# Optimization experiments

Hardware: AMD Instinct MI355X
Metric: run time of the kernel (lower is better)

## Reference

```python
import jax, jax.numpy as jnp
import numpy as np
from jax import lax

NUM_CHANNELS = 3
NUM_HEADS = 8
PATCH = 16  # projection_dim = 3 * 16 * 16 = 768
EPS = 1e-5


def setup_inputs() -> dict:
    key = jax.random.key(0)
    ks = jax.random.split(key, 16)
    B, N, D, Hdim = 4, 1024, 768, 3072
    H = NUM_HEADS

    def init(k, shape, fan_in):
        bound = 1.0 / np.sqrt(fan_in)
        return jax.random.uniform(k, shape, jnp.float32, -bound, bound)

    return {
        "x": jax.random.normal(ks[0], (B, N, D), jnp.float32),
        # 3x3 conv QKV projections over per-patch [3,16,16] images (no bias, qkv_bias=False)
        "qconv_w": init(ks[1], (NUM_CHANNELS, NUM_CHANNELS, 3, 3), NUM_CHANNELS * 9),
        "kconv_w": init(ks[2], (NUM_CHANNELS, NUM_CHANNELS, 3, 3), NUM_CHANNELS * 9),
        "vconv_w": init(ks[3], (NUM_CHANNELS, NUM_CHANNELS, 3, 3), NUM_CHANNELS * 9),
        # 1x1 conv mixing heads of the attention map + BatchNorm2d(heads)
        "reatten_w": init(ks[4], (H, H), H),
        "reatten_b": init(ks[5], (H,), H),
        "bn_g": jnp.ones((H,), jnp.float32),
        "bn_b": jnp.zeros((H,), jnp.float32),
        # output projection (Linear dim->dim)
        "proj_w": init(ks[6], (D, D), D),
        "proj_b": init(ks[7], (D,), D),
        # LayerNorm over (num_patches, projection_dim) jointly
        "ln_g": jnp.ones((N, D), jnp.float32),
        "ln_b": jnp.zeros((N, D), jnp.float32),
        # FeedForward
        "ff_w1": init(ks[8], (Hdim, D), D),
        "ff_b1": init(ks[9], (Hdim,), D),
        "ff_w2": init(ks[10], (D, Hdim), Hdim),
        "ff_b2": init(ks[11], (D,), Hdim),
    }


def _conv3x3(x, w):
    # x: [BN, C, p, p], w: [C, C, 3, 3], stride 1, SAME padding
    return lax.conv_general_dilated(x, w, (1, 1), "SAME",
                                    dimension_numbers=("NCHW", "OIHW", "NCHW"))


def _layernorm_2d(x, g, b):
    # LayerNorm over last two axes (N, D) jointly, biased variance, eps=1e-5
    mu = jnp.mean(x, axis=(-2, -1), keepdims=True)
    var = jnp.mean(jnp.square(x - mu), axis=(-2, -1), keepdims=True)
    return (x - mu) * lax.rsqrt(var + EPS) * g + b


def _encoder_fwd(x, qconv_w, kconv_w, vconv_w, reatten_w, reatten_b,
                 bn_g, bn_b, proj_w, proj_b, ln_g, ln_b,
                 ff_w1, ff_b1, ff_w2, ff_b2):
    B, N, D = x.shape
    H = NUM_HEADS
    hd = D // H
    scale = hd ** -0.5

    # --- ReAttention ---
    xi = x.reshape(B * N, NUM_CHANNELS, PATCH, PATCH)

    def qkv(w):
        y = _conv3x3(xi, w).reshape(B, N, H, hd)
        return y.transpose(0, 2, 1, 3)  # [B, H, N, hd]

    q, k, v = qkv(qconv_w), qkv(kconv_w), qkv(vconv_w)

    attn = jax.nn.softmax(jnp.einsum("bhnd,bhmd->bhnm", q, k) * scale, axis=-1)

    # learned cross-head 1x1 conv + BatchNorm2d (training-mode batch stats)
    attn = jnp.einsum("gh,bhnm->bgnm", reatten_w, attn) + reatten_b[None, :, None, None]
    mu = jnp.mean(attn, axis=(0, 2, 3), keepdims=True)
    var = jnp.mean(jnp.square(attn - mu), axis=(0, 2, 3), keepdims=True)
    attn = (attn - mu) * lax.rsqrt(var + EPS)
    attn = attn * bn_g[None, :, None, None] + bn_b[None, :, None, None]

    out = jnp.einsum("bhnm,bhmd->bhnd", attn, v)
    out = out.transpose(0, 2, 1, 3).reshape(B, N, D)
    out = out @ proj_w.T + proj_b

    # --- residual + LN ---
    x1 = _layernorm_2d(x + out, ln_g, ln_b)

    # --- FeedForward (exact GELU) + residual + LN ---
    h = jax.nn.gelu(x1 @ ff_w1.T + ff_b1, approximate=False)
    ff = h @ ff_w2.T + ff_b2
    return _layernorm_2d(x1 + ff, ln_g, ln_b)


def reference(x, qconv_w, kconv_w, vconv_w, reatten_w, reatten_b,
              bn_g, bn_b, proj_w, proj_b, ln_g, ln_b,
              ff_w1, ff_b1, ff_w2, ff_b2):
    return _encoder_fwd(x, qconv_w, kconv_w, vconv_w, reatten_w, reatten_b,
                        bn_g, bn_b, proj_w, proj_b, ln_g, ln_b,
                        ff_w1, ff_b1, ff_w2, ff_b2)
```

## Files before the change

kernel.cpp:

```cpp
#include <hip/hip_runtime.h>
#include <math.h>


typedef unsigned short u16;
typedef unsigned int u32;
typedef __bf16 bf16x8 __attribute__((ext_vector_type(8)));
typedef float f32x4 __attribute__((ext_vector_type(4)));

#define EPSV 1e-5f
#define SL2E 0.14724444620253177f
#define EXPC -11.541560327111707f

__device__ __forceinline__ u16 f2bf(float f) {
  union { float f; u32 u; } v; v.f = f;
  u32 u = v.u + 0x7fffu + ((v.u >> 16) & 1u);
  return (u16)(u >> 16);
}
__device__ __forceinline__ float bf2f(u16 h) {
  union { u32 u; float f; } v; v.u = ((u32)h) << 16; return v.f;
}
__device__ __forceinline__ f32x4 mfma16(bf16x8 a, bf16x8 b, f32x4 c) {
  return __builtin_amdgcn_mfma_f32_16x16x32_bf16(a, b, c, 0, 0, 0);
}
__device__ __forceinline__ void gload16(const void* gp, void* lp) {
  __builtin_amdgcn_global_load_lds(
      (const __attribute__((address_space(1))) u32*)gp,
      (__attribute__((address_space(3))) u32*)lp, 16, 0, 0);
}

struct KS { int off[3]; int hl[3]; };
__device__ __forceinline__ KS ks_init(int t) {
  KS ks;
  int lane = t & 63;
  int lh = lane >> 4, l15 = lane & 15;
  #pragma unroll
  for (int j = 0; j < 3; ++j) {
    int G = j * 512 + t;
    int hl = (G >= 768) ? 1 : 0;
    int C = (G - hl * 768) >> 6;
    int chunk = C / 6, r = C - 6 * chunk;
    int kk = r >> 1, c1 = r & 1;
    int m = chunk * 32 + ((l15 >> 2) << 3) + (c1 << 2) + (l15 & 3);
    ks.off[j] = m * 96 + kk * 32 + lh * 8;
    ks.hl[j] = hl;
  }
  return ks;
}
__device__ __forceinline__ void ks_stage(const u16* __restrict__ khi,
    const u16* __restrict__ klo, size_t rowel, const KS& ks, u16* Kb, int t) {
  int w = t >> 6;
  #pragma unroll
  for (int j = 0; j < 3; ++j) {
    const u16* src = (ks.hl[j] ? klo : khi) + rowel + ks.off[j];
    gload16(src, Kb + (size_t)(j * 512 + w * 64) * 8);
  }
}

__device__ __forceinline__ void qload(const u16* __restrict__ qhi,
    const u16* __restrict__ qlo, size_t qoff, bf16x8* qh, bf16x8* ql) {
  #pragma unroll
  for (int kk = 0; kk < 3; ++kk) {
    qh[kk] = *(const bf16x8*)(qhi + qoff + kk * 32);
    ql[kk] = *(const bf16x8*)(qlo + qoff + kk * 32);
  }
}

__device__ __forceinline__ void score18(const u16* Kb, int mh, int lane,
    const bf16x8* qh, const bf16x8* ql, f32x4& C0, f32x4& C1) {
  C0 = (f32x4){0.f, 0.f, 0.f, 0.f};
  C1 = (f32x4){0.f, 0.f, 0.f, 0.f};
  #pragma unroll
  for (int kk = 0; kk < 3; ++kk) {
    const u16* base = Kb + (mh * 6 + kk * 2) * 512 + lane * 8;
    bf16x8 kh0 = *(const bf16x8*)(base);
    bf16x8 kh1 = *(const bf16x8*)(base + 512);
    bf16x8 kl0 = *(const bf16x8*)(base + 6144);
    bf16x8 kl1 = *(const bf16x8*)(base + 6656);
    C0 = mfma16(kh0, qh[kk], C0);
    C0 = mfma16(kl0, qh[kk], C0);
    C0 = mfma16(kh0, ql[kk], C0);
    C1 = mfma16(kh1, qh[kk], C1);
    C1 = mfma16(kl1, qh[kk], C1);
    C1 = mfma16(kh1, ql[kk], C1);
  }
}

__global__ __launch_bounds__(256) void k_f2b(const float* __restrict__ s,
                                             u16* __restrict__ d, int n) {
  int i = blockIdx.x * 256 + threadIdx.x;
  int stride = gridDim.x * 256;
  for (; i < n; i += stride) d[i] = f2bf(s[i]);
}

__global__ __launch_bounds__(256) void k_conv(const float* __restrict__ x,
    const float* __restrict__ wq, const float* __restrict__ wk, const float* __restrict__ wv,
    u16* __restrict__ qhi, u16* __restrict__ qlo,
    u16* __restrict__ khi, u16* __restrict__ klo,
    float* __restrict__ vb)
{
  __shared__ float patch[768], swq[81], swk[81], swv[81];
  int bid = blockIdx.x;
  int b = bid >> 10, n = bid & 1023;
  int t = threadIdx.x;
  const float* xr = x + (size_t)bid * 768;
  patch[t] = xr[t]; patch[t + 256] = xr[t + 256]; patch[t + 512] = xr[t + 512];
  if (t < 81) { swq[t] = wq[t]; swk[t] = wk[t]; swv[t] = wv[t]; }
  __syncthreads();
  #pragma unroll
  for (int r = 0; r < 3; ++r) {
    int f = t + 256 * r;
    int o = f >> 8, rem = f & 255, pp = rem >> 4, qq = rem & 15;
    float aq = 0.f, ak = 0.f, av = 0.f;
    #pragma unroll
    for (int i = 0; i < 3; ++i)
      #pragma unroll
      for (int dp = 0; dp < 3; ++dp) {
        int ip = pp + dp - 1;
        if (ip < 0 || ip > 15) continue;
        #pragma unroll
        for (int dq = 0; dq < 3; ++dq) {
          int iq = qq + dq - 1;
          if (iq < 0 || iq > 15) continue;
          float pv = patch[i * 256 + ip * 16 + iq];
          int wi = ((o * 3 + i) * 3 + dp) * 3 + dq;
          aq += swq[wi] * pv; ak += swk[wi] * pv; av += swv[wi] * pv;
        }
      }
    int h = f / 96, d = f - h * 96;
    size_t oi = ((size_t)(b * 8 + h) * 1024 + n) * 96 + d;
    float aqs = aq * SL2E;
    u16 qh_ = f2bf(aqs); qhi[oi] = qh_; qlo[oi] = f2bf(aqs - bf2f(qh_));
    u16 kh_ = f2bf(ak);  khi[oi] = kh_; klo[oi] = f2bf(ak - bf2f(kh_));
    vb[oi] = av;
  }
}

__global__ __launch_bounds__(256) void k_vtr(const float* __restrict__ vb,
                                             u16* __restrict__ vtr)
{
  __shared__ u16 lds[12288];
  int bid = blockIdx.x;
  int bh = bid >> 3, n0 = (bid & 7) * 128;
  int t = threadIdx.x;
  int n = t >> 1, dh = (t & 1) * 48;
  const float* src = vb + ((size_t)bh * 1024 + n0 + n) * 96 + dh;
  #pragma unroll
  for (int j4 = 0; j4 < 12; ++j4) {
    float4 v = *(const float4*)(src + j4 * 4);
    int d = dh + j4 * 4;
    lds[(d + 0) * 128 + n] = f2bf(v.x);
    lds[(d + 1) * 128 + n] = f2bf(v.y);
    lds[(d + 2) * 128 + n] = f2bf(v.z);
    lds[(d + 3) * 128 + n] = f2bf(v.w);
  }
  __syncthreads();
  #pragma unroll
  for (int j = 0; j < 48; ++j) {
    int flat = t + 256 * j;
    int d = flat >> 7, n2 = flat & 127;
    vtr[((size_t)bh * 96 + d) * 1024 + n0 + n2] = lds[flat];
  }
}

__global__ __launch_bounds__(512, 2) void k_score(
    const u16* __restrict__ qhi, const u16* __restrict__ qlo,
    const u16* __restrict__ khi, const u16* __restrict__ klo,
    float* __restrict__ zp, u16* __restrict__ pt)
{
  __shared__ u16 Kst[2][12288];
  int p = blockIdx.x;
  int s = p >> 3;
  int c = (p & 7) * 4 + (s >> 4);
  int ng = s & 15;
  int b = c >> 3, mg = c & 7;
  int t = threadIdx.x, lane = t & 63, w = t >> 6;
  int l15 = lane & 15, lhi = lane >> 4;
  int nsub = w >> 1, mh = w & 1;
  int n0 = ng * 64 + nsub * 16;
  int nt = ng * 4 + nsub;
  int m0base = mg * 128;
  KS ks = ks_init(t);
  bf16x8 qh[3], ql[3], qh2[3], ql2[3];
  size_t bh0 = (size_t)(b * 8) * 1024;
  ks_stage(khi, klo, (bh0 + m0base) * 96, ks, Kst[0], t);
  qload(qhi, qlo, (bh0 + n0 + l15) * 96 + lhi * 8, qh, ql);
  __syncthreads();
  #pragma unroll 1
  for (int h = 0; h < 8; ++h) {
    float z = 0.f;
    #pragma unroll
    for (int mt = 0; mt < 2; ++mt) {
      int u = h * 2 + mt;
      if (u < 15) {
        int un = u + 1, hn = un >> 1, mtn = un & 1;
        size_t bhn = (size_t)(b * 8 + hn) * 1024;
        ks_stage(khi, klo, (bhn + m0base + mtn * 64) * 96, ks, Kst[(u + 1) & 1], t);
        if (mtn == 0)
          qload(qhi, qlo, (bhn + n0 + l15) * 96 + lhi * 8, qh2, ql2);
      }
      f32x4 C0, C1;
      score18(Kst[u & 1], mh, lane, qh, ql, C0, C1);
      union { u16 us[8]; uint4 q4; } pk;
      #pragma unroll
      for (int r = 0; r < 4; ++r) {
        float e0 = exp2f(C0[r] + EXPC);
        float e1 = exp2f(C1[r] + EXPC);
        z += e0 + e1;
        pk.us[r]     = f2bf(e0);
        pk.us[4 + r] = f2bf(e1);
      }
      int mc = mg * 4 + mt * 2 + mh;
      *(uint4*)&pt[((((size_t)(b * 8 + h) * 32 + mc) * 64 + nt) * 64 + lane) * 8] = pk.q4;
      if (u < 15 && mt == 1) {
        #pragma unroll
        for (int kk = 0; kk < 3; ++kk) { qh[kk] = qh2[kk]; ql[kk] = ql2[kk]; }
      }
      __syncthreads();
    }
    z += __shfl_xor(z, 16);
    z += __shfl_xor(z, 32);
    if (lane < 16)
      zp[((size_t)((b * 8 + h) * 16 + mg * 2 + mh)) * 1024 + n0 + lane] = z;
  }
}

__global__ __launch_bounds__(256) void k_zmerge(const float* __restrict__ zp,
                                                float* __restrict__ invZ)
{
  int idx = blockIdx.x * 256 + threadIdx.x;
  int bh = idx >> 10, n = idx & 1023;
  float z = 0.f;
  #pragma unroll
  for (int s = 0; s < 16; ++s) z += zp[((size_t)(bh * 16 + s)) * 1024 + n];
  invZ[idx] = 1.f / z;
}

__global__ __launch_bounds__(256, 4) void k_mix(
    u16* __restrict__ pt, const float* __restrict__ invZ,
    const float* __restrict__ rw, float* __restrict__ pstat)
{
  __shared__ float red[4][16];
  int t = threadIdx.x;
  int gid = blockIdx.x * 256 + t;
  int lane = gid & 63;
  int nt = (gid >> 6) & 63;
  int mc = (gid >> 12) & 31;
  int b  = gid >> 17;
  int n = nt * 16 + (lane & 15);
  float iz[8];
  #pragma unroll
  for (int h = 0; h < 8; ++h) iz[h] = invZ[(b * 8 + h) * 1024 + n];
  float out[8][8];
  #pragma unroll
  for (int g = 0; g < 8; ++g) {
    float wsum = 0.f;
    #pragma unroll
    for (int h = 0; h < 8; ++h) wsum += rw[g * 8 + h];
    float cg = -wsum * (1.f / 1024.f);
    #pragma unroll
    for (int e = 0; e < 8; ++e) out[g][e] = cg;
  }
  size_t base = ((((size_t)(b * 8) * 32 + mc) * 64 + nt) * 64 + lane) * 8;
  #pragma unroll
  for (int h = 0; h < 8; ++h) {
    union { u32 ud[4]; uint4 q; } gr;
    gr.q = *(const uint4*)(pt + base + (size_t)h * 1048576);
    float q[8];
    #pragma unroll
    for (int k2 = 0; k2 < 4; ++k2) {
      union { u32 u; float f; } lo, hi;
      lo.u = gr.ud[k2] << 16;
      hi.u = gr.ud[k2] & 0xffff0000u;
      q[2 * k2]     = lo.f * iz[h];
      q[2 * k2 + 1] = hi.f * iz[h];
    }
    #pragma unroll
    for (int g = 0; g < 8; ++g) {
      float wgh = rw[g * 8 + h];
      #pragma unroll
      for (int e = 0; e < 8; ++e) out[g][e] += wgh * q[e];
    }
  }
  float sc[8], scc[8];
  #pragma unroll
  for (int g = 0; g < 8; ++g) {
    float s = 0.f, ss = 0.f;
    union { u16 us[8]; uint4 q; } pk;
    #pragma unroll
    for (int e = 0; e < 8; ++e) {
      float v = out[g][e];
      s += v; ss += v * v;
      pk.us[e] = f2bf(v);
    }
    sc[g] = s; scc[g] = ss;
    *(uint4*)(pt + base + (size_t)g * 1048576) = pk.q;
  }
  int wv = t >> 6, lane2 = t & 63;
  #pragma unroll
  for (int off = 32; off > 0; off >>= 1)
    #pragma unroll
    for (int g = 0; g < 8; ++g) {
      sc[g] += __shfl_down(sc[g], off);
      scc[g] += __shfl_down(scc[g], off);
    }
  if (lane2 == 0) {
    #pragma unroll
    for (int g = 0; g < 8; ++g) {
      red[wv][g] = sc[g];
      red[wv][8 + g] = scc[g];
    }
  }
  __syncthreads();
  if (t < 16)
    pstat[(size_t)blockIdx.x * 16 + t] =
        red[0][t] + red[1][t] + red[2][t] + red[3][t];
}

__global__ __launch_bounds__(256, 4) void k_pv(
    const u16* __restrict__ pt, const u16* __restrict__ vtr,
    float* __restrict__ U)
{
  int p = blockIdx.x;
  int t = threadIdx.x, lane = t & 63, w = t >> 6;
  int l15 = lane & 15, lhi = lane >> 4;
  int xcd = p & 7;
  int i = p >> 3;
  int pair = xcd * 4 + (i >> 4);
  int ntq = i & 15;
  int b = pair >> 3, g = pair & 7;
  int nt = ntq * 4 + w;
  f32x4 acc[6];
  #pragma unroll
  for (int ds = 0; ds < 6; ++ds) acc[ds] = (f32x4){0.f, 0.f, 0.f, 0.f};
  size_t pbase = ((((size_t)(b * 8 + g) * 32) * 64 + nt) * 64 + lane);
  size_t vbase = (size_t)(b * 8 + g) * 96;
  #pragma unroll 2
  for (int mc = 0; mc < 32; ++mc) {
    bf16x8 pf = *(const bf16x8*)(pt + (pbase + (size_t)mc * 4096) * 8);
    int mof = mc * 32 + lhi * 8;
    #pragma unroll
    for (int ds = 0; ds < 6; ++ds) {
      bf16x8 vf = *(const bf16x8*)(vtr + (vbase + ds * 16 + l15) * 1024 + mof);
      acc[ds] = mfma16(pf, vf, acc[ds]);
    }
  }
  #pragma unroll
  for (int ds = 0; ds < 6; ++ds)
    #pragma unroll
    for (int r = 0; r < 4; ++r) {
      int n = nt * 16 + lhi * 4 + r;
      U[((size_t)(b * 1024 + n)) * 768 + g * 96 + ds * 16 + l15] = acc[ds][r];
    }
}

__global__ __launch_bounds__(384) void k_vcs(const float* __restrict__ vb,
                                             float* __restrict__ vcs)
{
  __shared__ float part[4][96];
  int bh = blockIdx.x, t = threadIdx.x;
  int c = t % 96, g4 = t / 96;
  float a = 0.f;
  const float* vp = vb + (size_t)bh * 98304 + (size_t)g4 * 24576 + c;
  for (int m = 0; m < 256; ++m) a += vp[m * 96];
  part[g4][c] = a;
  __syncthreads();
  if (t < 96) vcs[bh * 96 + t] = part[0][t] + part[1][t] + part[2][t] + part[3][t];
}

__global__ __launch_bounds__(256) void k_statred(const float* __restrict__ pstat,
                                                 float* __restrict__ stats)
{
  __shared__ float part[16][17];
  int t = threadIdx.x;
  int j = t >> 4, s = t & 15;
  float a = 0.f;
  for (int k2 = 0; k2 < 128; ++k2)
    a += pstat[(size_t)(s + 16 * k2) * 16 + j];
  part[j][s] = a;
  __syncthreads();
  if (t < 16) {
    float v = 0.f;
    #pragma unroll
    for (int s2 = 0; s2 < 16; ++s2) v += part[t][s2];
    stats[t] = v;
  }
}

__global__ __launch_bounds__(256) void k_bnfin(const float* __restrict__ U,
    const float* __restrict__ vcs, const float* __restrict__ stats,
    const float* __restrict__ bng, const float* __restrict__ bnb,
    u16* __restrict__ ubb)
{
  size_t idx = (size_t)blockIdx.x * 256 + threadIdx.x;
  int col = (int)(idx % 768); int i = (int)(idx / 768); int b = i >> 10;
  int g = col / 96, d = col - g * 96;
  const float cnt = 4194304.f;
  float mc = stats[g] / cnt;
  float var = stats[8 + g] / cnt - mc * mc;
  float sg = bng[g] * rsqrtf(var + EPSV);
  float tg = bnb[g] - sg * mc;
  ubb[idx] = f2bf(sg * U[idx] + tg * vcs[(b * 8 + g) * 96 + d]);
}

template<int GELU_, int RES_, int STATS_, int BF16OUT>
__global__ __launch_bounds__(256) void k_gemm(
    const u16* __restrict__ A, const u16* __restrict__ W,
    const float* __restrict__ bias, const float* __restrict__ res,
    float* __restrict__ out, u16* __restrict__ outb,
    int K, int Nc, float* __restrict__ stats)
{
  __shared__ u16 As[8192], Bs[8192];
  __shared__ float red[8];
  int t = threadIdx.x, lane = t & 63, wv = t >> 6;
  int l15 = lane & 15, lhi = lane >> 4;
  int i0 = blockIdx.y * 128, j0 = blockIdx.x * 128;
  int wr = wv >> 1, wc = wv & 1;
  f32x4 acc[4][4];
  #pragma unroll
  for (int mi = 0; mi < 4; ++mi)
    #pragma unroll
    for (int ni = 0; ni < 4; ++ni) acc[mi][ni] = (f32x4){0.f, 0.f, 0.f, 0.f};
  int rA = lane >> 3;
  int colel = 8 * ((lane & 7) ^ rA);
  for (int k0 = 0; k0 < K; k0 += 64) {
    if (k0) __syncthreads();
    #pragma unroll
    for (int i = 0; i < 4; ++i) {
      int cA = wv * 4 + i;
      int r = cA * 8 + rA;
      gload16(A + (size_t)(i0 + r) * K + k0 + colel, &As[cA * 512]);
      gload16(W + (size_t)(j0 + r) * K + k0 + colel, &Bs[cA * 512]);
    }
    __syncthreads();
    #pragma unroll
    for (int ks = 0; ks < 2; ++ks) {
      bf16x8 af[4], bf[4];
      #pragma unroll
      for (int mi = 0; mi < 4; ++mi) {
        int r2 = wr * 64 + mi * 16 + l15;
        af[mi] = *(const bf16x8*)&As[r2 * 64 + ((ks * 32 + lhi * 8) ^ (8 * (r2 & 7)))];
      }
      #pragma unroll
      for (int ni = 0; ni < 4; ++ni) {
        int r3 = wc * 64 + ni * 16 + l15;
        bf[ni] = *(const bf16x8*)&Bs[r3 * 64 + ((ks * 32 + lhi * 8) ^ (8 * (r3 & 7)))];
      }
      #pragma unroll
      for (int mi = 0; mi < 4; ++mi)
        #pragma unroll
        for (int ni = 0; ni < 4; ++ni)
          acc[mi][ni] = mfma16(af[mi], bf[ni], acc[mi][ni]);
    }
  }
  float ls = 0.f, lss = 0.f;
  #pragma unroll
  for (int mi = 0; mi < 4; ++mi) {
    #pragma unroll
    for (int ni = 0; ni < 4; ++ni) {
      int col = j0 + wc * 64 + ni * 16 + l15;
      float bv = bias[col];
      #pragma unroll
      for (int r = 0; r < 4; ++r) {
        int row = i0 + wr * 64 + mi * 16 + lhi * 4 + r;
        float val = acc[mi][ni][r] + bv;
        if (RES_) val += res[(size_t)row * Nc + col];
        if (GELU_) val = 0.5f * val * (1.f + erff(val * 0.70710678118654752f));
        if (BF16OUT) outb[(size_t)row * Nc + col] = f2bf(val);
        else out[(size_t)row * Nc + col] = val;
        if (STATS_) { ls += val; lss += val * val; }
      }
    }
  }
  if (STATS_) {
    #pragma unroll
    for (int off = 32; off > 0; off >>= 1) {
      ls += __shfl_down(ls, off); lss += __shfl_down(lss, off);
    }
    if (lane == 0) { red[wv * 2] = ls; red[wv * 2 + 1] = lss; }
    __syncthreads();
    if (t == 0) {
      int b = i0 >> 10;
      atomicAdd(&stats[b * 2],     red[0] + red[2] + red[4] + red[6]);
      atomicAdd(&stats[b * 2 + 1], red[1] + red[3] + red[5] + red[7]);
    }
  }
}

template<int BF16OUT>
__global__ __launch_bounds__(256) void k_ln(const float* __restrict__ y,
    const float* __restrict__ stats, const float* __restrict__ g,
    const float* __restrict__ bta, float* __restrict__ outp, u16* __restrict__ outb)
{
  size_t idx = (size_t)blockIdx.x * 256 + threadIdx.x;
  int i = (int)(idx / 768), col = (int)(idx % 768);
  int b = i >> 10, n = i & 1023;
  const float cnt = 786432.f;
  float mu = stats[b * 2] / cnt;
  float var = stats[b * 2 + 1] / cnt - mu * mu;
  float r = rsqrtf(var + EPSV);
  size_t gi = (size_t)n * 768 + col;
  float v = (y[idx] - mu) * r * g[gi] + bta[gi];
  outp[idx] = v;
  if (BF16OUT) outb[idx] = f2bf(v);
}

extern "C" void kernel_launch(void* const* d_in, const int* in_sizes, int n_in,
                              void* d_out, int out_size, void* d_ws, size_t ws_size,
                              hipStream_t stream)
{
  const float* x   = (const float*)d_in[0];
  const float* qw  = (const float*)d_in[1];
  const float* kw  = (const float*)d_in[2];
  const float* vw  = (const float*)d_in[3];
  const float* rw  = (const float*)d_in[4];
  const float* bng = (const float*)d_in[6];
  const float* bnb = (const float*)d_in[7];
  const float* pw  = (const float*)d_in[8];
  const float* pb  = (const float*)d_in[9];
  const float* lng = (const float*)d_in[10];
  const float* lnb = (const float*)d_in[11];
  const float* fw1 = (const float*)d_in[12];
  const float* fb1 = (const float*)d_in[13];
  const float* fw2 = (const float*)d_in[14];
  const float* fb2 = (const float*)d_in[15];
  float* out = (float*)d_out;

  u16* pt   = (u16*)d_ws;
  float* vb = (float*)pt;
  u16* hb   = pt;
  float* y2 = (float*)pt + 12582912;
  float* fsm = (float*)(pt + 33554432);
  float* stats = fsm;
  float* pstat = fsm + 64;
  float* vcs   = fsm + 32832;
  float* zp    = fsm + 35904;
  float* invZ  = fsm + 560192;
  u16* qhi  = (u16*)(fsm + 592960);
  u16* qlo  = qhi + 3145728;
  u16* khi  = qlo + 3145728;
  u16* klo  = khi + 3145728;
  u16* vtrb = klo + 3145728;
  u16* pwb  = vtrb + 3145728;
  u16* fw1b = pwb + 589824;
  u16* fw2b = fw1b + 2359296;
  float* U0 = (float*)qhi;
  float* x1 = (float*)khi;
  float* y1 = U0;
  u16* ubb  = vtrb;
  u16* x1b  = vtrb;

  hipMemsetAsync(stats, 0, 64 * sizeof(float), stream);
  k_f2b<<<1024, 256, 0, stream>>>(pw, pwb, 589824);
  k_f2b<<<2048, 256, 0, stream>>>(fw1, fw1b, 2359296);
  k_f2b<<<2048, 256, 0, stream>>>(fw2, fw2b, 2359296);

  k_conv<<<4096, 256, 0, stream>>>(x, qw, kw, vw, qhi, qlo, khi, klo, vb);
  k_vtr<<<256, 256, 0, stream>>>(vb, vtrb);
  k_vcs<<<32, 384, 0, stream>>>(vb, vcs);
  k_score<<<512, 512, 0, stream>>>(qhi, qlo, khi, klo, zp, pt);
  k_zmerge<<<128, 256, 0, stream>>>(zp, invZ);
  k_mix<<<2048, 256, 0, stream>>>(pt, invZ, rw, pstat);
  k_pv<<<512, 256, 0, stream>>>(pt, vtrb, U0);
  k_statred<<<1, 256, 0, stream>>>(pstat, stats);
  k_bnfin<<<12288, 256, 0, stream>>>(U0, vcs, stats, bng, bnb, ubb);

  k_gemm<0,1,1,0><<<dim3(6, 32), 256, 0, stream>>>(ubb, pwb, pb, x, y1, nullptr, 768, 768, stats + 16);
  k_ln<1><<<12288, 256, 0, stream>>>(y1, stats + 16, lng, lnb, x1, x1b);
  k_gemm<1,0,0,1><<<dim3(24, 32), 256, 0, stream>>>(x1b, fw1b, fb1, nullptr, nullptr, hb, 768, 3072, nullptr);
  k_gemm<0,1,1,0><<<dim3(6, 32), 256, 0, stream>>>(hb, fw2b, fb2, x1, y2, nullptr, 3072, 768, stats + 24);
  k_ln<0><<<12288, 256, 0, stream>>>(y2, stats + 24, lng, lnb, out, nullptr);
}
```

Measured before the change: 367.4 us.

## Split k_mix work per thread in half and split-K the PV reduction

k_mix now handles 4 elements per thread instead of 8 and launches twice as many blocks, which cuts register pressure and raises parallelism; pstat and the stat reduction are resized to match. k_pv splits the m-loop into two halves written to separate U0/U1 buffers, doubling the grid to 1024 blocks, and k_bnfin sums both partial buffers. This targets underutilised CUs in these kernels, at the cost of extra U traffic in bnfin and more partial stats to reduce.

```diff
diff --git a/kernel.cpp b/kernel.cpp
--- a/kernel.cpp
+++ b/kernel.cpp
@@ -235,22 +235,23 @@
   invZ[idx] = 1.f / z;
 }
 
-__global__ __launch_bounds__(256, 4) void k_mix(
+__global__ __launch_bounds__(256) void k_mix(
     u16* __restrict__ pt, const float* __restrict__ invZ,
     const float* __restrict__ rw, float* __restrict__ pstat)
 {
   __shared__ float red[4][16];
   int t = threadIdx.x;
   int gid = blockIdx.x * 256 + t;
-  int lane = gid & 63;
-  int nt = (gid >> 6) & 63;
-  int mc = (gid >> 12) & 31;
-  int b  = gid >> 17;
+  int half = gid & 1;
+  int lane = (gid >> 1) & 63;
+  int nt = (gid >> 7) & 63;
+  int mc = (gid >> 13) & 31;
+  int b  = gid >> 18;
   int n = nt * 16 + (lane & 15);
   float iz[8];
   #pragma unroll
   for (int h = 0; h < 8; ++h) iz[h] = invZ[(b * 8 + h) * 1024 + n];
-  float out[8][8];
+  float out[8][4];
   #pragma unroll
   for (int g = 0; g < 8; ++g) {
     float wsum = 0.f;
@@ -258,42 +259,38 @@
     for (int h = 0; h < 8; ++h) wsum += rw[g * 8 + h];
     float cg = -wsum * (1.f / 1024.f);
     #pragma unroll
-    for (int e = 0; e < 8; ++e) out[g][e] = cg;
-  }
-  size_t base = ((((size_t)(b * 8) * 32 + mc) * 64 + nt) * 64 + lane) * 8;
+    for (int e = 0; e < 4; ++e) out[g][e] = cg;
+  }
+  size_t base = ((((size_t)(b * 8) * 32 + mc) * 64 + nt) * 64 + lane) * 8 + half * 4;
   #pragma unroll
   for (int h = 0; h < 8; ++h) {
-    union { u32 ud[4]; uint4 q; } gr;
-    gr.q = *(const uint4*)(pt + base + (size_t)h * 1048576);
-    float q[8];
-    #pragma unroll
-    for (int k2 = 0; k2 < 4; ++k2) {
-      union { u32 u; float f; } lo, hi;
-      lo.u = gr.ud[k2] << 16;
-      hi.u = gr.ud[k2] & 0xffff0000u;
-      q[2 * k2]     = lo.f * iz[h];
-      q[2 * k2 + 1] = hi.f * iz[h];
-    }
+    uint2 gr = *(const uint2*)(pt + base + (size_t)h * 1048576);
+    float izh = iz[h];
+    union { u32 u; float f; } c0, c1, c2, c3;
+    c0.u = gr.x << 16;
+    c1.u = gr.x & 0xffff0000u;
+    c2.u = gr.y << 16;
+    c3.u = gr.y & 0xffff0000u;
+    float q0 = c0.f * izh, q1 = c1.f * izh, q2 = c2.f * izh, q3 = c3.f * izh;
     #pragma unroll
     for (int g = 0; g < 8; ++g) {
       float wgh = rw[g * 8 + h];
-      #pragma unroll
-      for (int e = 0; e < 8; ++e) out[g][e] += wgh * q[e];
+      out[g][0] += wgh * q0;
+      out[g][1] += wgh * q1;
+      out[g][2] += wgh * q2;
+      out[g][3] += wgh * q3;
     }
   }
   float sc[8], scc[8];
   #pragma unroll
   for (int g = 0; g < 8; ++g) {
-    float s = 0.f, ss = 0.f;
-    union { u16 us[8]; uint4 q; } pk;
-    #pragma unroll
-    for (int e = 0; e < 8; ++e) {
-      float v = out[g][e];
-      s += v; ss += v * v;
-      pk.us[e] = f2bf(v);
-    }
-    sc[g] = s; scc[g] = ss;
-    *(uint4*)(pt + base + (size_t)g * 1048576) = pk.q;
+    float o0 = out[g][0], o1 = out[g][1], o2 = out[g][2], o3 = out[g][3];
+    sc[g] = (o0 + o1) + (o2 + o3);
+    scc[g] = (o0 * o0 + o1 * o1) + (o2 * o2 + o3 * o3);
+    uint2 pk;
+    pk.x = (u32)f2bf(o0) | ((u32)f2bf(o1) << 16);
+    pk.y = (u32)f2bf(o2) | ((u32)f2bf(o3) << 16);
+    *(uint2*)(pt + base + (size_t)g * 1048576) = pk;
   }
   int wv = t >> 6, lane2 = t & 63;
   #pragma unroll
@@ -318,15 +315,16 @@
 
 __global__ __launch_bounds__(256, 4) void k_pv(
     const u16* __restrict__ pt, const u16* __restrict__ vtr,
-    float* __restrict__ U)
+    float* __restrict__ U0, float* __restrict__ U1)
 {
   int p = blockIdx.x;
   int t = threadIdx.x, lane = t & 63, w = t >> 6;
   int l15 = lane & 15, lhi = lane >> 4;
   int xcd = p & 7;
   int i = p >> 3;
-  int pair = xcd * 4 + (i >> 4);
-  int ntq = i & 15;
+  int pair = xcd * 4 + (i >> 5);
+  int rest = i & 31;
+  int ntq = rest >> 1, mhf = rest & 1;
   int b = pair >> 3, g = pair & 7;
   int nt = ntq * 4 + w;
   f32x4 acc[6];
@@ -335,7 +333,7 @@
   size_t pbase = ((((size_t)(b * 8 + g) * 32) * 64 + nt) * 64 + lane);
   size_t vbase = (size_t)(b * 8 + g) * 96;
   #pragma unroll 2
-  for (int mc = 0; mc < 32; ++mc) {
+  for (int mc = mhf * 16; mc < mhf * 16 + 16; ++mc) {
     bf16x8 pf = *(const bf16x8*)(pt + (pbase + (size_t)mc * 4096) * 8);
     int mof = mc * 32 + lhi * 8;
     #pragma unroll
@@ -344,12 +342,13 @@
       acc[ds] = mfma16(pf, vf, acc[ds]);
     }
   }
+  float* Uq = mhf ? U1 : U0;
   #pragma unroll
   for (int ds = 0; ds < 6; ++ds)
     #pragma unroll
     for (int r = 0; r < 4; ++r) {
       int n = nt * 16 + lhi * 4 + r;
-      U[((size_t)(b * 1024 + n)) * 768 + g * 96 + ds * 16 + l15] = acc[ds][r];
+      Uq[((size_t)(b * 1024 + n)) * 768 + g * 96 + ds * 16 + l15] = acc[ds][r];
     }
 }
 
@@ -374,7 +373,7 @@
   int t = threadIdx.x;
   int j = t >> 4, s = t & 15;
   float a = 0.f;
-  for (int k2 = 0; k2 < 128; ++k2)
+  for (int k2 = 0; k2 < 256; ++k2)
     a += pstat[(size_t)(s + 16 * k2) * 16 + j];
   part[j][s] = a;
   __syncthreads();
@@ -386,10 +385,10 @@
   }
 }
 
-__global__ __launch_bounds__(256) void k_bnfin(const float* __restrict__ U,
-    const float* __restrict__ vcs, const float* __restrict__ stats,
-    const float* __restrict__ bng, const float* __restrict__ bnb,
-    u16* __restrict__ ubb)
+__global__ __launch_bounds__(256) void k_bnfin(const float* __restrict__ U0,
+    const float* __restrict__ U1, const float* __restrict__ vcs,
+    const float* __restrict__ stats, const float* __restrict__ bng,
+    const float* __restrict__ bnb, u16* __restrict__ ubb)
 {
   size_t idx = (size_t)blockIdx.x * 256 + threadIdx.x;
   int col = (int)(idx % 768); int i = (int)(idx / 768); int b = i >> 10;
@@ -399,7 +398,7 @@
   float var = stats[8 + g] / cnt - mc * mc;
   float sg = bng[g] * rsqrtf(var + EPSV);
   float tg = bnb[g] - sg * mc;
-  ubb[idx] = f2bf(sg * U[idx] + tg * vcs[(b * 8 + g) * 96 + d]);
+  ubb[idx] = f2bf(sg * (U0[idx] + U1[idx]) + tg * vcs[(b * 8 + g) * 96 + d]);
 }
 
 template<int GELU_, int RES_, int STATS_, int BF16OUT>
@@ -532,10 +531,10 @@
   float* fsm = (float*)(pt + 33554432);
   float* stats = fsm;
   float* pstat = fsm + 64;
-  float* vcs   = fsm + 32832;
-  float* zp    = fsm + 35904;
-  float* invZ  = fsm + 560192;
-  u16* qhi  = (u16*)(fsm + 592960);
+  float* vcs   = fsm + 65600;
+  float* zp    = fsm + 68672;
+  float* invZ  = fsm + 592960;
+  u16* qhi  = (u16*)(fsm + 625728);
   u16* qlo  = qhi + 3145728;
   u16* khi  = qlo + 3145728;
   u16* klo  = khi + 3145728;
@@ -544,6 +543,7 @@
   u16* fw1b = pwb + 589824;
   u16* fw2b = fw1b + 2359296;
   float* U0 = (float*)qhi;
+  float* U1 = (float*)khi;
   float* x1 = (float*)khi;
   float* y1 = U0;
   u16* ubb  = vtrb;
@@ -559,10 +559,10 @@
   k_vcs<<<32, 384, 0, stream>>>(vb, vcs);
   k_score<<<512, 512, 0, stream>>>(qhi, qlo, khi, klo, zp, pt);
   k_zmerge<<<128, 256, 0, stream>>>(zp, invZ);
-  k_mix<<<2048, 256, 0, stream>>>(pt, invZ, rw, pstat);
-  k_pv<<<512, 256, 0, stream>>>(pt, vtrb, U0);
+  k_mix<<<4096, 256, 0, stream>>>(pt, invZ, rw, pstat);
+  k_pv<<<1024, 256, 0, stream>>>(pt, vtrb, U0, U1);
   k_statred<<<1, 256, 0, stream>>>(pstat, stats);
-  k_bnfin<<<12288, 256, 0, stream>>>(U0, vcs, stats, bng, bnb, ubb);
+  k_bnfin<<<12288, 256, 0, stream>>>(U0, U1, vcs, stats, bng, bnb, ubb);
 
   k_gemm<0,1,1,0><<<dim3(6, 32), 256, 0, stream>>>(ubb, pwb, pb, x, y1, nullptr, 768, 768, stats + 16);
   k_ln<1><<<12288, 256, 0, stream>>>(y1, stats + 16, lng, lnb, x1, x1b);
```

After: 336.8 us. -8.3%, faster.
